# Performance work log

Hardware: AMD Instinct MI355X
Metric: run time of the kernel (lower is better)

## Reference

```python
import jax, jax.numpy as jnp
import numpy as np

B, T, D, H = 2048, 2048, 3, 32  # batch, time steps, input_size, hidden_size


def setup_inputs() -> dict:
    key = jax.random.key(0)
    k0, k1, k2, k3, k4 = jax.random.split(key, 5)
    lim = 1.0 / np.sqrt(H)  # eqx.nn.GRUCell init range
    inp = jax.random.normal(k0, (B, T, D), dtype=jnp.float32)
    weight_ih = jax.random.uniform(k1, (3 * H, D), minval=-lim, maxval=lim, dtype=jnp.float32)
    weight_hh = jax.random.uniform(k2, (3 * H, H), minval=-lim, maxval=lim, dtype=jnp.float32)
    bias = jax.random.uniform(k3, (3 * H,), minval=-lim, maxval=lim, dtype=jnp.float32)
    bias_n = jax.random.uniform(k4, (H,), minval=-lim, maxval=lim, dtype=jnp.float32)
    return {"inp": inp, "weight_ih": weight_ih, "weight_hh": weight_hh,
            "bias": bias, "bias_n": bias_n}


def reference(inp, weight_ih, weight_hh, bias, bias_n):
    # inp: [B, T, D]. Faithful batched version of PinnWithGRU.__call__:
    # scan an eqx.nn.GRUCell over time from a zero hidden state, output hidden[0] per step.
    b = inp.shape[0]
    h0 = jnp.zeros((b, H), dtype=inp.dtype)
    xs = jnp.swapaxes(inp, 0, 1)  # [T, B, D]

    def step(h, x):
        ig = x @ weight_ih.T + bias      # [B, 3H] input gates (+ bias, as in eqx)
        hg = h @ weight_hh.T             # [B, 3H] hidden gates
        ir, iz, ia = jnp.split(ig, 3, axis=-1)
        hr, hz, ha = jnp.split(hg, 3, axis=-1)
        r = jax.nn.sigmoid(ir + hr)
        z = jax.nn.sigmoid(iz + hz)
        n = jnp.tanh(ia + bias_n + r * ha)
        h_new = (1.0 - z) * n + z * h
        return h_new, h_new[:, 0]        # emit first hidden unit per step

    _, out = jax.lax.scan(step, h0, xs)  # out: [T, B]
    return jnp.swapaxes(out, 0, 1)[..., None]  # [B, T, 1] (matches per-seq [T, 1])
```

## Files before the change

kernel.cpp:

```cpp
#include <hip/hip_runtime.h>


#define GRU_B 2048
#define GRU_T 2048
#define GRU_D 3
#define GRU_H 32
#define CHUNK 32

#define WAIT_LGKM0 0xC07F

__device__ __forceinline__ float fast_sigmoid(float x) {
    float e = __expf(-x);
    return __builtin_amdgcn_rcpf(1.0f + e);
}
__device__ __forceinline__ float fast_tanh(float x) {
    float e = __expf(2.0f * x);
    return 1.0f - 2.0f * __builtin_amdgcn_rcpf(e + 1.0f);
}
__device__ __forceinline__ float xor32(float v, int paddr) {
    return __int_as_float(__builtin_amdgcn_ds_bpermute(paddr, __float_as_int(v)));
}

__global__ __launch_bounds__(64, 2) void gru_scan_kernel(
    const float* __restrict__ inp,
    const float* __restrict__ w_ih,
    const float* __restrict__ w_hh,
    const float* __restrict__ bias,
    const float* __restrict__ bias_n,
    float* __restrict__ out)
{
    __shared__ __align__(16) float h2[4 * GRU_H];
    __shared__ __align__(16) float x_lds[CHUNK * GRU_D];

    const int lane  = threadIdx.x;
    const int unit  = lane & 31;
    const int half  = lane >> 5;
    const int b     = blockIdx.x;
    const int paddr = (lane ^ 32) << 2;

    const int rowA = unit + 32 * half;
    const int rowB = unit + 32 * (1 - half);
    const int rowC = 2 * GRU_H + unit;
    const int kofs = 16 * half;

    float wa[16], wb[16], wc[16];
    {
        const float4* pa = (const float4*)(w_hh + (size_t)rowA * GRU_H + kofs);
        const float4* pb = (const float4*)(w_hh + (size_t)rowB * GRU_H + kofs);
        const float4* pc = (const float4*)(w_hh + (size_t)rowC * GRU_H + kofs);
#pragma unroll
        for (int q = 0; q < 4; ++q) {
            float4 A = pa[q], Bv = pb[q], Cv = pc[q];
            wa[4*q+0]=A.x;  wa[4*q+1]=A.y;  wa[4*q+2]=A.z;  wa[4*q+3]=A.w;
            wb[4*q+0]=Bv.x; wb[4*q+1]=Bv.y; wb[4*q+2]=Bv.z; wb[4*q+3]=Bv.w;
            wc[4*q+0]=Cv.x; wc[4*q+1]=Cv.y; wc[4*q+2]=Cv.z; wc[4*q+3]=Cv.w;
        }
    }
    float wia[GRU_D], wic[GRU_D];
#pragma unroll
    for (int d = 0; d < GRU_D; ++d) {
        wia[d] = w_ih[(size_t)rowA * GRU_D + d];
        wic[d] = w_ih[(size_t)rowC * GRU_D + d];
    }
    const float bA = bias[rowA];
    const float bC = bias[rowC] + bias_n[unit];

    const float* xb = inp + (size_t)b * GRU_T * GRU_D;
    float*       ob = out + (size_t)b * GRU_T;

    float h = 0.0f;
    float outreg = 0.0f;

    h2[lane] = 0.0f;
    __builtin_amdgcn_s_waitcnt(WAIT_LGKM0);

    const float4* hv = (const float4*)(h2 + 48 * half);
    const int wbase = unit + 64 * half;

    for (int c = 0; c < GRU_T / CHUNK; ++c) {
        {
            const int base = c * (CHUNK * GRU_D);
            x_lds[lane] = xb[base + lane];
            if (lane < CHUNK * GRU_D - 64) x_lds[64 + lane] = xb[base + 64 + lane];
        }
        __builtin_amdgcn_s_waitcnt(WAIT_LGKM0);

#pragma unroll 8
        for (int s = 0; s < CHUNK; ++s) {
            float hk[16];
#pragma unroll
            for (int q = 0; q < 4; ++q) {
                float4 v = hv[q];
                hk[4*q+0]=v.x; hk[4*q+1]=v.y; hk[4*q+2]=v.z; hk[4*q+3]=v.w;
            }
            const float x0 = x_lds[3 * s + 0];
            const float x1 = x_lds[3 * s + 1];
            const float x2 = x_lds[3 * s + 2];

            const float aM = fmaf(wia[2], x2, fmaf(wia[1], x1, fmaf(wia[0], x0, bA)));
            const float aN = fmaf(wic[2], x2, fmaf(wic[1], x1, fmaf(wic[0], x0, bC)));

            float A = 0.0f, Bp = 0.0f, Cp = 0.0f;
#pragma unroll
            for (int k = 0; k < 16; ++k) {
                A  = fmaf(wa[k], hk[k], A);
                Bp = fmaf(wb[k], hk[k], Bp);
                Cp = fmaf(wc[k], hk[k], Cp);
            }
            const float gM = A  + xor32(Bp, paddr);
            const float gN = Cp + xor32(Cp, paddr);

            const float sg  = fast_sigmoid(aM + gM);
            const float zsw = xor32(sg, paddr);
            const float n   = fast_tanh(fmaf(sg, gN, aN));
            const float hnew = fmaf(zsw, h - n, n);

            if (lane == s - 1) outreg = hk[0];

            h = hnew;
            h2[wbase]      = h;
            h2[wbase + 32] = h;
            __builtin_amdgcn_s_waitcnt(WAIT_LGKM0);
        }

        {
            const float h0 = h2[0];
            if (lane == CHUNK - 1) outreg = h0;
        }
        if (lane < CHUNK) ob[c * CHUNK + lane] = outreg;
    }
}

extern "C" void kernel_launch(void* const* d_in, const int* in_sizes, int n_in,
                              void* d_out, int out_size, void* d_ws, size_t ws_size,
                              hipStream_t stream) {
    const float* inp    = (const float*)d_in[0];
    const float* w_ih   = (const float*)d_in[1];
    const float* w_hh   = (const float*)d_in[2];
    const float* bias   = (const float*)d_in[3];
    const float* bias_n = (const float*)d_in[4];
    float* out = (float*)d_out;

    dim3 grid(GRU_B);
    dim3 block(64);
    gru_scan_kernel<<<grid, block, 0, stream>>>(inp, w_ih, w_hh, bias, bias_n, out);
}
```

Measured before the change: 708.2 us.

## Use permlane32 swap for half-wave exchange and read inputs from global

Replaces the ds_bpermute half-wave exchanges with the permlane32_swap builtin when it is available, so the partner-half values no longer go through LDS. Each step now writes the hidden state to LDS once instead of twice, with a new layout where the low and high halves each read their own 16-element slice. The per-chunk staging of x into LDS is removed: inputs are read straight from global memory, which the compiler can turn into uniform scalar loads. CHUNK drops to 16 with a fully unrolled inner loop. The intent is to shorten the latency-bound serial step chain; the high half now computes a hidden value that is never read, which is harmless but relies on the new layout being right.

After: 756.2 us. 6.8% more time.

```diff
diff --git a/kernel.cpp b/kernel.cpp
--- a/kernel.cpp
+++ b/kernel.cpp
@@ -5,7 +5,7 @@
 #define GRU_T 2048
 #define GRU_D 3
 #define GRU_H 32
-#define CHUNK 32
+#define CHUNK 16
 
 #define WAIT_LGKM0 0xC07F
 
@@ -17,9 +17,23 @@
     float e = __expf(2.0f * x);
     return 1.0f - 2.0f * __builtin_amdgcn_rcpf(e + 1.0f);
 }
-__device__ __forceinline__ float xor32(float v, int paddr) {
+
+#if __has_builtin(__builtin_amdgcn_permlane32_swap)
+#define HAVE_PLSWAP 1
+typedef int v2i __attribute__((ext_vector_type(2)));
+__device__ __forceinline__ void bcast_halves(float v, float& lo_b, float& hi_b) {
+    v2i r = __builtin_amdgcn_permlane32_swap(__float_as_int(v), __float_as_int(v),
+                                             false, false);
+    lo_b = __int_as_float(r.x);
+    hi_b = __int_as_float(r.y);
+}
+#else
+#define HAVE_PLSWAP 0
+__device__ __forceinline__ float xor32(float v) {
+    int paddr = (int)((threadIdx.x ^ 32u) << 2);
     return __int_as_float(__builtin_amdgcn_ds_bpermute(paddr, __float_as_int(v)));
 }
+#endif
 
 __global__ __launch_bounds__(64, 2) void gru_scan_kernel(
     const float* __restrict__ inp,
@@ -29,14 +43,13 @@
     const float* __restrict__ bias_n,
     float* __restrict__ out)
 {
-    __shared__ __align__(16) float h2[4 * GRU_H];
-    __shared__ __align__(16) float x_lds[CHUNK * GRU_D];
+    __shared__ __align__(16) float h2[96];
 
     const int lane  = threadIdx.x;
     const int unit  = lane & 31;
     const int half  = lane >> 5;
     const int b     = blockIdx.x;
-    const int paddr = (lane ^ 32) << 2;
+    const bool lo32 = (lane < 32);
 
     const int rowA = unit + 32 * half;
     const int rowB = unit + 32 * (1 - half);
@@ -71,21 +84,16 @@
     float h = 0.0f;
     float outreg = 0.0f;
 
-    h2[lane] = 0.0f;
+    h2[lane < 32 ? lane : 32 + lane] = 0.0f;
     __builtin_amdgcn_s_waitcnt(WAIT_LGKM0);
 
-    const float4* hv = (const float4*)(h2 + 48 * half);
+    const float4* hv = (const float4*)(h2 + kofs);
     const int wbase = unit + 64 * half;
 
     for (int c = 0; c < GRU_T / CHUNK; ++c) {
-        {
-            const int base = c * (CHUNK * GRU_D);
-            x_lds[lane] = xb[base + lane];
-            if (lane < CHUNK * GRU_D - 64) x_lds[64 + lane] = xb[base + 64 + lane];
-        }
-        __builtin_amdgcn_s_waitcnt(WAIT_LGKM0);
+        const float* xs = xb + c * (CHUNK * GRU_D);
 
-#pragma unroll 8
+#pragma unroll
         for (int s = 0; s < CHUNK; ++s) {
             float hk[16];
 #pragma unroll
@@ -93,9 +101,9 @@
                 float4 v = hv[q];
                 hk[4*q+0]=v.x; hk[4*q+1]=v.y; hk[4*q+2]=v.z; hk[4*q+3]=v.w;
             }
-            const float x0 = x_lds[3 * s + 0];
-            const float x1 = x_lds[3 * s + 1];
-            const float x2 = x_lds[3 * s + 2];
+            const float x0 = xs[3 * s + 0];
+            const float x1 = xs[3 * s + 1];
+            const float x2 = xs[3 * s + 2];
 
             const float aM = fmaf(wia[2], x2, fmaf(wia[1], x1, fmaf(wia[0], x0, bA)));
             const float aN = fmaf(wic[2], x2, fmaf(wic[1], x1, fmaf(wic[0], x0, bC)));
@@ -107,19 +115,32 @@
                 Bp = fmaf(wb[k], hk[k], Bp);
                 Cp = fmaf(wc[k], hk[k], Cp);
             }
-            const float gM = A  + xor32(Bp, paddr);
-            const float gN = Cp + xor32(Cp, paddr);
 
-            const float sg  = fast_sigmoid(aM + gM);
-            const float zsw = xor32(sg, paddr);
-            const float n   = fast_tanh(fmaf(sg, gN, aN));
-            const float hnew = fmaf(zsw, h - n, n);
+#if HAVE_PLSWAP
+            float cLo, cHi;
+            bcast_halves(Cp, cLo, cHi);
+            const float gN = cLo + cHi;
+            float bLo, bHi;
+            bcast_halves(Bp, bLo, bHi);
+            const float gM = aM + A + (lo32 ? bHi : bLo);
+            const float sg = fast_sigmoid(gM);
+            float sLo, sHi;
+            bcast_halves(sg, sLo, sHi);
+            const float zg = sHi;
+#else
+            const float gN = Cp + xor32(Cp);
+            const float gM = aM + A + xor32(Bp);
+            const float sg = fast_sigmoid(gM);
+            const float zg = lo32 ? xor32(sg) : sg;
+#endif
+
+            const float n    = fast_tanh(fmaf(sg, gN, aN));
+            const float hnew = fmaf(zg, h - n, n);
 
             if (lane == s - 1) outreg = hk[0];
 
             h = hnew;
-            h2[wbase]      = h;
-            h2[wbase + 32] = h;
+            h2[wbase] = h;
             __builtin_amdgcn_s_waitcnt(WAIT_LGKM0);
         }
 
```
